# Kernel optimization log

Hardware: AMD Instinct MI355X
Metric: run time of the kernel (lower is better)

Reference implementation:

```python
import jax, jax.numpy as jnp
import numpy as np

VOCAB = 4096
CODE_DIM = 3
DECAY = 0.99
EPS = 1e-05


def setup_inputs() -> dict:
    key = jax.random.key(0)
    k1, k2, k3, k4 = jax.random.split(key, 4)
    feats = jax.random.normal(k1, (4, 8192, CODE_DIM), dtype=jnp.float32)
    embed = jax.random.normal(k2, (VOCAB, CODE_DIM), dtype=jnp.float32)
    ema_cluster_size = jax.random.uniform(k3, (VOCAB,), dtype=jnp.float32)
    ema_weight = jax.random.normal(k4, (VOCAB, CODE_DIM), dtype=jnp.float32)
    return {"feats": feats, "embed": embed,
            "ema_cluster_size": ema_cluster_size, "ema_weight": ema_weight}


def reference(feats, embed, ema_cluster_size, ema_weight):
    B, L, D = feats.shape
    flat = feats.reshape(-1, D)  # (N, D)
    # squared-euclidean distances to all codes: (N, V)
    dist = (jnp.sum(flat * flat, axis=1, keepdims=True)
            - 2.0 * flat @ embed.T
            + jnp.sum(embed * embed, axis=1))
    idx = jnp.argmin(dist, axis=1)  # (N,)
    quant = embed[idx].reshape(B, L, D)

    # EMA codebook update (training mode), done with segment_sum instead of a
    # dense (N, V) one-hot matmul -- same math.
    counts = jax.ops.segment_sum(jnp.ones_like(flat[:, 0]), idx, num_segments=VOCAB)
    sums = jax.ops.segment_sum(flat, idx, num_segments=VOCAB)  # (V, D)
    new_cluster_size = DECAY * ema_cluster_size + (1.0 - DECAY) * counts
    new_ema_weight = DECAY * ema_weight + (1.0 - DECAY) * sums
    n = jnp.sum(new_cluster_size)
    cluster_size = (new_cluster_size + EPS) / (n + VOCAB * EPS) * n
    new_embed = new_ema_weight / cluster_size[:, None]

    # VQ loss with stop-gradients matching torch detach semantics
    loss = (jnp.mean((quant - jax.lax.stop_gradient(feats)) ** 2)
            + 0.25 * jnp.mean((feats - jax.lax.stop_gradient(quant)) ** 2))
    # straight-through estimator
    quant_st = feats + jax.lax.stop_gradient(quant - feats)
    return (quant_st, idx.reshape(B, L), loss,
            new_cluster_size, new_ema_weight, new_embed)
```

## Files before the change

### kernel.cpp

```cpp
#include <hip/hip_runtime.h>
#include <math.h>

#pragma clang fp contract(off)

#define VOCAB 4096
#define NPTS  32768
#define NELEM 98304
#define BLOCK 1024
#define NWAVE 16
#define CPW   (VOCAB / NWAVE)
#define PAIRS_PW (CPW / 2)
#define PPL   2
#define PTS_PER_BLOCK (64 * PPL)

typedef float v2f __attribute__((ext_vector_type(2)));

__global__ __launch_bounds__(1024) void vq_prep(
    const float* __restrict__ embed, float4* __restrict__ pc)
{
  const int m = blockIdx.x * 1024 + threadIdx.x;
  const int c0 = 2 * m, c1 = 2 * m + 1;
  float a0 = embed[3 * c0 + 0], a1 = embed[3 * c0 + 1], a2 = embed[3 * c0 + 2];
  float b0 = embed[3 * c1 + 0], b1 = embed[3 * c1 + 1], b2 = embed[3 * c1 + 2];
  float esqa = (a0 * a0 + a1 * a1) + a2 * a2;
  float esqb = (b0 * b0 + b1 * b1) + b2 * b2;
  pc[2 * m + 0] = make_float4(-(a0 + a0), -(b0 + b0), -(a1 + a1), -(b1 + b1));
  pc[2 * m + 1] = make_float4(-(a2 + a2), -(b2 + b2), esqa, esqb);
}

#define EVALPAIR(P0, P1, C2, ST)                                              \
  {                                                                           \
    v2f A  = {(P0).x, (P0).y};                                                \
    v2f Bv = {(P0).z, (P0).w};                                                \
    v2f Cv = {(P1).x, (P1).y};                                                \
    v2f Sv = {(P1).z, (P1).w};                                                \
    _Pragma("unroll")                                                         \
    for (int s = 0; s < PPL; ++s) {                                           \
      v2f t;                                                                  \
      asm("v_pk_mul_f32 %0, %1, %2" : "=v"(t) : "v"(xp0[s]), "v"(A));         \
      asm("v_pk_fma_f32 %0, %1, %2, %0" : "+v"(t) : "v"(xp1[s]), "v"(Bv));    \
      asm("v_pk_fma_f32 %0, %1, %2, %0" : "+v"(t) : "v"(xp2[s]), "v"(Cv));    \
      asm("v_pk_add_f32 %0, %1, %0" : "+v"(t) : "v"(xpq[s]));                 \
      asm("v_pk_add_f32 %0, %1, %0" : "+v"(t) : "v"(Sv));                     \
      if (t.x < bst[ST][s])     { bst[ST][s] = t.x;     bix[ST][s] = (C2); }  \
      if (t.y < bst[(ST)+1][s]) { bst[(ST)+1][s] = t.y; bix[(ST)+1][s] = (C2) + 1; } \
    }                                                                         \
  }

__global__ __launch_bounds__(BLOCK, 4) void vq_assign(
    const float* __restrict__ feats, const float* __restrict__ embed,
    const float4* __restrict__ gpc,
    float* __restrict__ out_quant, float* __restrict__ out_idx,
    float* __restrict__ counts, float* __restrict__ sums,
    float* __restrict__ sse)
{
  extern __shared__ float4 lpc[];
  __shared__ float dbuf[NWAVE][PPL][64];
  __shared__ int   ibuf[NWAVE][PPL][64];

  const int tid  = threadIdx.x;
  const int lane = tid & 63;
  const int wv   = tid >> 6;

  #pragma unroll
  for (int c = tid; c < 2 * (VOCAB / 2) * 2; c += BLOCK) lpc[c] = gpc[c];
  __syncthreads();

  const int pbase = blockIdx.x * PTS_PER_BLOCK;
  float px[PPL][3];
  v2f xp0[PPL], xp1[PPL], xp2[PPL], xpq[PPL];
  #pragma unroll
  for (int s = 0; s < PPL; ++s) {
    const int p = pbase + s * 64 + lane;
    float x0 = feats[3 * p + 0];
    float x1 = feats[3 * p + 1];
    float x2 = feats[3 * p + 2];
    px[s][0] = x0; px[s][1] = x1; px[s][2] = x2;
    float xsq = (x0 * x0 + x1 * x1) + x2 * x2;
    xp0[s] = (v2f){x0, x0}; xp1[s] = (v2f){x1, x1};
    xp2[s] = (v2f){x2, x2}; xpq[s] = (v2f){xsq, xsq};
  }

  float bst[4][PPL];
  int   bix[4][PPL];
  #pragma unroll
  for (int st = 0; st < 4; ++st)
    #pragma unroll
    for (int s = 0; s < PPL; ++s) { bst[st][s] = INFINITY; bix[st][s] = 0; }

  const int mbase = wv * PAIRS_PW;
  int vz;
  asm volatile("v_mov_b32 %0, 0" : "=v"(vz));
  const float4* gpcv = gpc + vz;

  #pragma unroll 2
  for (int j = 0; j < PAIRS_PW; j += 2) {
    const int m0 = mbase + j;
    const int m1 = m0 + 1;
    float4 L0 = lpc[2 * m0 + 0];
    float4 L1 = lpc[2 * m0 + 1];
    float4 G0 = gpcv[2 * m1 + 0];
    float4 G1 = gpcv[2 * m1 + 1];
    EVALPAIR(L0, L1, 2 * m0, 0);
    EVALPAIR(G0, G1, 2 * m1, 2);
  }

  #pragma unroll
  for (int s = 0; s < PPL; ++s) {
    float b = bst[0][s];
    int   bi = bix[0][s];
    #pragma unroll
    for (int st = 1; st < 4; ++st) {
      if (bst[st][s] < b || (bst[st][s] == b && bix[st][s] < bi)) {
        b = bst[st][s]; bi = bix[st][s];
      }
    }
    dbuf[wv][s][lane] = b;
    ibuf[wv][s][lane] = bi;
  }
  __syncthreads();

  if (wv == 0) {
    #pragma unroll
    for (int s = 0; s < PPL; ++s) {
      float b = dbuf[0][s][lane];
      int   bi = ibuf[0][s][lane];
      #pragma unroll
      for (int w = 1; w < NWAVE; ++w) {
        float od = dbuf[w][s][lane];
        int   oi = ibuf[w][s][lane];
        if (od < b || (od == b && oi < bi)) { b = od; bi = oi; }
      }

      const int p = pbase + s * 64 + lane;
      const float q0 = embed[3 * bi + 0];
      const float q1 = embed[3 * bi + 1];
      const float q2 = embed[3 * bi + 2];
      const float x0 = px[s][0], x1 = px[s][1], x2 = px[s][2];

      out_quant[3 * p + 0] = x0 + (q0 - x0);
      out_quant[3 * p + 1] = x1 + (q1 - x1);
      out_quant[3 * p + 2] = x2 + (q2 - x2);
      out_idx[p] = (float)bi;

      atomicAdd(&counts[bi], 1.0f);
      atomicAdd(&sums[3 * bi + 0], x0);
      atomicAdd(&sums[3 * bi + 1], x1);
      atomicAdd(&sums[3 * bi + 2], x2);

      float d0 = q0 - x0, d1 = q1 - x1, d2 = q2 - x2;
      float l = (d0 * d0 + d1 * d1) + d2 * d2;
      #pragma unroll
      for (int m = 1; m <= 32; m <<= 1) l += __shfl_xor(l, m, 64);
      if (lane == 0) atomicAdd(sse, l);
    }
  }
}

__global__ __launch_bounds__(1024) void vq_ema(
    const float* __restrict__ counts, const float* __restrict__ sums,
    const float* __restrict__ sse,
    const float* __restrict__ ema_cs, const float* __restrict__ ema_w,
    float* __restrict__ out_loss, float* __restrict__ out_ncs,
    float* __restrict__ out_nw, float* __restrict__ out_nemb)
{
  __shared__ float part[16];
  const int tid = threadIdx.x;
  const float DEC = 0.99f;
  const float OMD = (float)(1.0 - 0.99);
  const float EPS = 1e-5f;

  float ncs[4];
  float nw[12];
  float nsum = 0.0f;

  #pragma unroll
  for (int k = 0; k < 4; ++k) {
    int v = k * 1024 + tid;
    float t = DEC * ema_cs[v] + OMD * counts[v];
    ncs[k] = t;
    out_ncs[v] = t;
    nsum += t;
    #pragma unroll
    for (int d = 0; d < 3; ++d) {
      float w = DEC * ema_w[3 * v + d] + OMD * sums[3 * v + d];
      nw[3 * k + d] = w;
      out_nw[3 * v + d] = w;
    }
  }

  #pragma unroll
  for (int m = 1; m <= 32; m <<= 1) nsum += __shfl_xor(nsum, m, 64);
  if ((tid & 63) == 0) part[tid >> 6] = nsum;
  __syncthreads();

  float n = 0.0f;
  #pragma unroll
  for (int i = 0; i < 16; ++i) n += part[i];
  const float denom = n + (float)VOCAB * EPS;

  #pragma unroll
  for (int k = 0; k < 4; ++k) {
    int v = k * 1024 + tid;
    float cs = (ncs[k] + EPS) / denom * n;
    #pragma unroll
    for (int d = 0; d < 3; ++d)
      out_nemb[3 * v + d] = nw[3 * k + d] / cs;
  }

  if (tid == 0) {
    float m = sse[0] / (float)NELEM;
    out_loss[0] = m + 0.25f * m;
  }
}

extern "C" void kernel_launch(void* const* d_in, const int* in_sizes, int n_in,
                              void* d_out, int out_size, void* d_ws, size_t ws_size,
                              hipStream_t stream) {
  const float* feats  = (const float*)d_in[0];
  const float* embed  = (const float*)d_in[1];
  const float* ema_cs = (const float*)d_in[2];
  const float* ema_w  = (const float*)d_in[3];

  float* out      = (float*)d_out;
  float* o_quant  = out;
  float* o_idx    = out + 98304;
  float* o_loss   = out + 131072;
  float* o_ncs    = out + 131073;
  float* o_nw     = out + 135169;
  float* o_nemb   = out + 147457;

  float*  ws_f      = (float*)d_ws;
  float*  ws_counts = ws_f;
  float*  ws_sums   = ws_f + 4096;
  float*  ws_sse    = ws_f + 16384;
  float4* ws_pc     = (float4*)(ws_f + 16388);

  hipMemsetAsync(d_ws, 0, (size_t)16385 * sizeof(float), stream);

  vq_prep<<<(VOCAB / 2) / 1024, 1024, 0, stream>>>(embed, ws_pc);

  vq_assign<<<NPTS / PTS_PER_BLOCK, BLOCK, VOCAB * sizeof(float4), stream>>>(
      feats, embed, ws_pc, o_quant, o_idx, ws_counts, ws_sums, ws_sse);

  vq_ema<<<1, 1024, 0, stream>>>(
      ws_counts, ws_sums, ws_sse, ema_cs, ema_w,
      o_loss, o_ncs, o_nw, o_nemb);
}
```

Before: 55.68 us.

## Software-pipeline codebook loads, halve LDS footprint, fold workspace memset into prep

Replaces the hipMemsetAsync with zeroing done inside vq_prep, which removes one launch. In vq_assign, only the pairs evaluated from LDS are staged there, so shared memory drops to 32 KB. The dbuf/ibuf reduction buffers now alias that same LDS after an extra barrier. The main loop becomes a four-stage rotating register pipeline that issues the LDS and global loads several iterations ahead of their use, hiding load latency at the cost of more VGPRs. This risks register spilling or lower occupancy under the 1024x4 launch bound.

```diff
diff --git a/kernel.cpp b/kernel.cpp
--- a/kernel.cpp
+++ b/kernel.cpp
@@ -10,15 +10,22 @@
 #define NWAVE 16
 #define CPW   (VOCAB / NWAVE)
 #define PAIRS_PW (CPW / 2)
+#define JITER (PAIRS_PW / 2)
 #define PPL   2
 #define PTS_PER_BLOCK (64 * PPL)
 
 typedef float v2f __attribute__((ext_vector_type(2)));
 
 __global__ __launch_bounds__(1024) void vq_prep(
-    const float* __restrict__ embed, float4* __restrict__ pc)
+    const float* __restrict__ embed, float4* __restrict__ pc,
+    float* __restrict__ wz)
 {
-  const int m = blockIdx.x * 1024 + threadIdx.x;
+  const int gid = blockIdx.x * 1024 + threadIdx.x;
+  #pragma unroll
+  for (int i = 0; i < 8; ++i) wz[gid * 8 + i] = 0.0f;
+  if (gid == 0) wz[16384] = 0.0f;
+
+  const int m = gid;
   const int c0 = 2 * m, c1 = 2 * m + 1;
   float a0 = embed[3 * c0 + 0], a1 = embed[3 * c0 + 1], a2 = embed[3 * c0 + 2];
   float b0 = embed[3 * c1 + 0], b1 = embed[3 * c1 + 1], b2 = embed[3 * c1 + 2];
@@ -47,6 +54,22 @@
     }                                                                         \
   }
 
+#define LOADS(S, jj)                                                          \
+  {                                                                           \
+    const int m0_ = mbase + 2 * (jj);                                         \
+    S##L0 = lpc[m0_];                                                         \
+    S##L1 = lpc[m0_ + 1];                                                     \
+    S##G0 = gpcv[2 * m0_ + 2];                                                \
+    S##G1 = gpcv[2 * m0_ + 3];                                                \
+  }
+
+#define COMP(S, jj)                                                           \
+  {                                                                           \
+    const int c2_ = 2 * (mbase + 2 * (jj));                                   \
+    EVALPAIR(S##L0, S##L1, c2_, 0);                                           \
+    EVALPAIR(S##G0, S##G1, c2_ + 2, 2);                                       \
+  }
+
 __global__ __launch_bounds__(BLOCK, 4) void vq_assign(
     const float* __restrict__ feats, const float* __restrict__ embed,
     const float4* __restrict__ gpc,
@@ -55,19 +78,17 @@
     float* __restrict__ sse)
 {
   extern __shared__ float4 lpc[];
-  __shared__ float dbuf[NWAVE][PPL][64];
-  __shared__ int   ibuf[NWAVE][PPL][64];
 
   const int tid  = threadIdx.x;
   const int lane = tid & 63;
   const int wv   = tid >> 6;
 
   #pragma unroll
-  for (int c = tid; c < 2 * (VOCAB / 2) * 2; c += BLOCK) lpc[c] = gpc[c];
+  for (int c = tid; c < 2048; c += BLOCK)
+    lpc[c] = gpc[4 * (c >> 1) + (c & 1)];
   __syncthreads();
 
   const int pbase = blockIdx.x * PTS_PER_BLOCK;
-  float px[PPL][3];
   v2f xp0[PPL], xp1[PPL], xp2[PPL], xpq[PPL];
   #pragma unroll
   for (int s = 0; s < PPL; ++s) {
@@ -75,7 +96,6 @@
     float x0 = feats[3 * p + 0];
     float x1 = feats[3 * p + 1];
     float x2 = feats[3 * p + 2];
-    px[s][0] = x0; px[s][1] = x1; px[s][2] = x2;
     float xsq = (x0 * x0 + x1 * x1) + x2 * x2;
     xp0[s] = (v2f){x0, x0}; xp1[s] = (v2f){x1, x1};
     xp2[s] = (v2f){x2, x2}; xpq[s] = (v2f){xsq, xsq};
@@ -93,18 +113,25 @@
   asm volatile("v_mov_b32 %0, 0" : "=v"(vz));
   const float4* gpcv = gpc + vz;
 
-  #pragma unroll 2
-  for (int j = 0; j < PAIRS_PW; j += 2) {
-    const int m0 = mbase + j;
-    const int m1 = m0 + 1;
-    float4 L0 = lpc[2 * m0 + 0];
-    float4 L1 = lpc[2 * m0 + 1];
-    float4 G0 = gpcv[2 * m1 + 0];
-    float4 G1 = gpcv[2 * m1 + 1];
-    EVALPAIR(L0, L1, 2 * m0, 0);
-    EVALPAIR(G0, G1, 2 * m1, 2);
-  }
-
+  float4 aL0, aL1, aG0, aG1;
+  float4 bL0, bL1, bG0, bG1;
+  float4 cL0, cL1, cG0, cG1;
+  float4 dL0, dL1, dG0, dG1;
+
+  LOADS(a, 0); LOADS(b, 1); LOADS(c, 2);
+  for (int jb = 0; jb < JITER - 4; jb += 4) {
+    LOADS(d, jb + 3); COMP(a, jb);
+    LOADS(a, jb + 4); COMP(b, jb + 1);
+    LOADS(b, jb + 5); COMP(c, jb + 2);
+    LOADS(c, jb + 6); COMP(d, jb + 3);
+  }
+  LOADS(d, JITER - 1);
+  COMP(a, JITER - 4); COMP(b, JITER - 3);
+  COMP(c, JITER - 2); COMP(d, JITER - 1);
+
+  __syncthreads();
+  float* dbuf = (float*)lpc;
+  int*   ibuf = (int*)lpc + NWAVE * PPL * 64;
   #pragma unroll
   for (int s = 0; s < PPL; ++s) {
     float b = bst[0][s];
@@ -115,20 +142,20 @@
         b = bst[st][s]; bi = bix[st][s];
       }
     }
-    dbuf[wv][s][lane] = b;
-    ibuf[wv][s][lane] = bi;
+    dbuf[(wv * PPL + s) * 64 + lane] = b;
+    ibuf[(wv * PPL + s) * 64 + lane] = bi;
   }
   __syncthreads();
 
   if (wv == 0) {
     #pragma unroll
     for (int s = 0; s < PPL; ++s) {
-      float b = dbuf[0][s][lane];
-      int   bi = ibuf[0][s][lane];
+      float b = dbuf[s * 64 + lane];
+      int   bi = ibuf[s * 64 + lane];
       #pragma unroll
       for (int w = 1; w < NWAVE; ++w) {
-        float od = dbuf[w][s][lane];
-        int   oi = ibuf[w][s][lane];
+        float od = dbuf[(w * PPL + s) * 64 + lane];
+        int   oi = ibuf[(w * PPL + s) * 64 + lane];
         if (od < b || (od == b && oi < bi)) { b = od; bi = oi; }
       }
 
@@ -136,7 +163,7 @@
       const float q0 = embed[3 * bi + 0];
       const float q1 = embed[3 * bi + 1];
       const float q2 = embed[3 * bi + 2];
-      const float x0 = px[s][0], x1 = px[s][1], x2 = px[s][2];
+      const float x0 = xp0[s].x, x1 = xp1[s].x, x2 = xp2[s].x;
 
       out_quant[3 * p + 0] = x0 + (q0 - x0);
       out_quant[3 * p + 1] = x1 + (q1 - x1);
@@ -236,11 +263,9 @@
   float*  ws_sse    = ws_f + 16384;
   float4* ws_pc     = (float4*)(ws_f + 16388);
 
-  hipMemsetAsync(d_ws, 0, (size_t)16385 * sizeof(float), stream);
-
-  vq_prep<<<(VOCAB / 2) / 1024, 1024, 0, stream>>>(embed, ws_pc);
-
-  vq_assign<<<NPTS / PTS_PER_BLOCK, BLOCK, VOCAB * sizeof(float4), stream>>>(
+  vq_prep<<<2, 1024, 0, stream>>>(embed, ws_pc, ws_f);
+
+  vq_assign<<<NPTS / PTS_PER_BLOCK, BLOCK, 2048 * sizeof(float4), stream>>>(
       feats, embed, ws_pc, o_quant, o_idx, ws_counts, ws_sums, ws_sse);
 
   vq_ema<<<1, 1024, 0, stream>>>(
```

Result: faster. 50.62 us (-9.1%).
